# Optimization experiments

Hardware: AMD Instinct MI355X
Metric: run time of the kernel (lower is better)

## Reference

```python
import jax, jax.numpy as jnp
import numpy as np

OUT_F, IN_F = 8192, 4096
TOKENS = 512


def _unpack_int2_to_ternary(packed, alpha, dtype):
    # packed: [out_f, in_f//4] ints 0..255; 4 two-bit codes per byte.
    # code 0 -> -1, code 2 -> +1, codes 1/3 -> 0; then scale by per-row alpha.
    shifts = jnp.arange(4, dtype=packed.dtype) * 2  # [0,2,4,6]
    two_bit = (packed[:, :, None] >> shifts[None, None, :]) & 3  # [out_f, in_f//4, 4]
    two_bit = two_bit.reshape(packed.shape[0], -1)  # [out_f, in_f]
    sign = jnp.where(two_bit == 2, 1.0, jnp.where(two_bit == 0, -1.0, 0.0)).astype(dtype)
    return sign * alpha.astype(dtype)[:, None]


def setup_inputs() -> dict:
    key = jax.random.key(0)
    k1, k2, k3, k4 = jax.random.split(key, 4)
    x = jax.random.normal(k1, (TOKENS, IN_F), dtype=jnp.float32)
    weight_int2 = jax.random.randint(k2, (OUT_F, IN_F // 4), 0, 256, dtype=jnp.int32)
    alpha = jax.random.uniform(k3, (OUT_F,), dtype=jnp.float32, minval=0.01, maxval=0.05)
    bias = jax.random.normal(k4, (OUT_F,), dtype=jnp.float32) * 0.01
    return {"x": x, "weight_int2": weight_int2, "alpha": alpha, "bias": bias}


def reference(x, weight_int2, alpha, bias):
    W = _unpack_int2_to_ternary(weight_int2, alpha, x.dtype)  # [out_f, in_f]
    out = x @ W.T  # [tokens, out_f]
    return out + bias
```

## Files before the change

kernel.cpp:

```cpp
#include <hip/hip_runtime.h>
#include <hip/hip_bf16.h>

typedef unsigned int u32;
typedef unsigned short u16;

#define TOKENS 512
#define OUT_F  8192
#define IN_F   4096
#define KPACK  (IN_F / 4)

#define TM 128
#define TN 64
#define BK 64
#define LDK 72

typedef __attribute__((ext_vector_type(8))) short bf16x8;
typedef __attribute__((ext_vector_type(4))) float f32x4;

__device__ __forceinline__ u32 pack_bf16x2(float a, float b) {
    __hip_bfloat162 h = __float22bfloat162_rn(make_float2(a, b));
    union { __hip_bfloat162 h2; u32 u; } cvt;
    cvt.h2 = h;
    return cvt.u;
}

__device__ __forceinline__ void decode4(u32 w, u32& lo, u32& hi) {
    u32 t = (w & 0xFFu) * 0x4001u;
    u32 u = t >> 4;
    u32 nt = ~t;
    u32 nu = ~u;
    lo = ((nt & 0x10001u) * 0x3F80u) | ((nt & 0x20002u) << 14);
    hi = ((nu & 0x10001u) * 0x3F80u) | ((nu & 0x20002u) << 14);
}

__global__ __launch_bounds__(256, 2) void ternary_gemm(
    const float* __restrict__ X,
    const u32* __restrict__ W2,
    const float* __restrict__ alpha,
    const float* __restrict__ bias,
    float* __restrict__ Out)
{
    __shared__ u16 As[TM * LDK];
    __shared__ u16 Bs[TN * LDK];

    const int tid  = threadIdx.x;
    const int lane = tid & 63;
    const int wave = tid >> 6;
    const int quad = lane >> 4;
    const int lr   = lane & 15;

    const int n0 = blockIdx.x * TN;
    const int m0 = blockIdx.y * TM;

    const int wm = (wave >> 1) * 64;
    const int wn = (wave & 1) * 32;

    f32x4 acc[4][2];
#pragma unroll
    for (int i = 0; i < 4; ++i)
#pragma unroll
        for (int j = 0; j < 2; ++j)
            acc[i][j] = (f32x4){0.f, 0.f, 0.f, 0.f};

    const int bn = tid >> 2;
    const int bq = tid & 3;

    float4 aregs[8];
    uint4 breg;

#pragma unroll
    for (int r = 0; r < 4; ++r) {
        int idx = r * 256 + tid;
        int m = idx >> 3, c = idx & 7;
        const float* p = X + (m0 + m) * IN_F + c * 8;
        aregs[2 * r]     = *(const float4*)(p);
        aregs[2 * r + 1] = *(const float4*)(p + 4);
    }
    breg = *(const uint4*)(W2 + (n0 + bn) * KPACK + bq * 4);

    for (int ks = 0; ks < IN_F; ks += BK) {
        __syncthreads();

#pragma unroll
        for (int r = 0; r < 4; ++r) {
            int idx = r * 256 + tid;
            int m = idx >> 3, c = idx & 7;
            float4 fa = aregs[2 * r], fb = aregs[2 * r + 1];
            uint4 q;
            q.x = pack_bf16x2(fa.x, fa.y);
            q.y = pack_bf16x2(fa.z, fa.w);
            q.z = pack_bf16x2(fb.x, fb.y);
            q.w = pack_bf16x2(fb.z, fb.w);
            *(uint4*)(As + m * LDK + c * 8) = q;
        }
        {
            u32 w0 = breg.x, w1 = breg.y, w2v = breg.z, w3 = breg.w;
            u32 o0, o1, o2, o3, o4, o5, o6, o7;
            decode4(w0, o0, o1);
            decode4(w1, o2, o3);
            decode4(w2v, o4, o5);
            decode4(w3, o6, o7);
            uint4 lo = {o0, o1, o2, o3};
            uint4 hi = {o4, o5, o6, o7};
            *(uint4*)(Bs + bn * LDK + bq * 16)     = lo;
            *(uint4*)(Bs + bn * LDK + bq * 16 + 8) = hi;
        }

        if (ks + BK < IN_F) {
            int ks2 = ks + BK;
#pragma unroll
            for (int r = 0; r < 4; ++r) {
                int idx = r * 256 + tid;
                int m = idx >> 3, c = idx & 7;
                const float* p = X + (m0 + m) * IN_F + ks2 + c * 8;
                aregs[2 * r]     = *(const float4*)(p);
                aregs[2 * r + 1] = *(const float4*)(p + 4);
            }
            breg = *(const uint4*)(W2 + (n0 + bn) * KPACK + (ks2 >> 2) + bq * 4);
        }

        __syncthreads();

#pragma unroll
        for (int kk = 0; kk < 2; ++kk) {
            bf16x8 afrag[4], bfrag[2];
#pragma unroll
            for (int mt = 0; mt < 4; ++mt)
                afrag[mt] = *(const bf16x8*)(As + (wm + mt * 16 + lr) * LDK + kk * 32 + quad * 8);
#pragma unroll
            for (int nt = 0; nt < 2; ++nt)
                bfrag[nt] = *(const bf16x8*)(Bs + (wn + nt * 16 + lr) * LDK + kk * 32 + quad * 8);
#pragma unroll
            for (int mt = 0; mt < 4; ++mt)
#pragma unroll
                for (int nt = 0; nt < 2; ++nt)
                    acc[mt][nt] = __builtin_amdgcn_mfma_f32_16x16x32_bf16(
                        afrag[mt], bfrag[nt], acc[mt][nt], 0, 0, 0);
        }
    }

#pragma unroll
    for (int nt = 0; nt < 2; ++nt) {
        int ncol = n0 + wn + nt * 16 + lr;
        float av = alpha[ncol];
        float bv = bias[ncol];
#pragma unroll
        for (int mt = 0; mt < 4; ++mt) {
            int mbase = m0 + wm + mt * 16 + quad * 4;
#pragma unroll
            for (int r = 0; r < 4; ++r) {
                Out[(mbase + r) * OUT_F + ncol] = acc[mt][nt][r] * av + bv;
            }
        }
    }
}

extern "C" void kernel_launch(void* const* d_in, const int* in_sizes, int n_in,
                              void* d_out, int out_size, void* d_ws, size_t ws_size,
                              hipStream_t stream) {
    const float* x = (const float*)d_in[0];
    const u32* w2 = (const u32*)d_in[1];
    const float* alpha = (const float*)d_in[2];
    const float* bias  = (const float*)d_in[3];
    float* out = (float*)d_out;

    dim3 grid(OUT_F / TN, TOKENS / TM);
    ternary_gemm<<<grid, 256, 0, stream>>>(x, w2, alpha, bias, out);
}
```

Before: 150.4 us.

## Drop LDS staging, load MFMA fragments from global, decode weights via LUT

Adds a pre-pass that converts X to bf16 in the workspace. The GEMM then loads A and B fragments directly from global memory into registers with double buffering, instead of staging them through shared memory with two barriers per k-step. Weight bytes are decoded through a 256-entry shared LUT rather than arithmetic. This removes the LDS round trips and synchronisation, but the direct global fragment loads are less coalesced, each operand is re-read by several waves rather than shared, and there is an extra kernel launch.

```diff
diff --git a/kernel.cpp b/kernel.cpp
--- a/kernel.cpp
+++ b/kernel.cpp
@@ -12,7 +12,6 @@
 #define TM 128
 #define TN 64
 #define BK 64
-#define LDK 72
 
 typedef __attribute__((ext_vector_type(8))) short bf16x8;
 typedef __attribute__((ext_vector_type(4))) float f32x4;
@@ -33,15 +32,29 @@
     hi = ((nu & 0x10001u) * 0x3F80u) | ((nu & 0x20002u) << 14);
 }
 
+__global__ __launch_bounds__(256) void convert_x(const float* __restrict__ X,
+                                                 u16* __restrict__ Xb) {
+    int i = (blockIdx.x * 256 + threadIdx.x) * 8;
+    float4 a = *(const float4*)(X + i);
+    float4 b = *(const float4*)(X + i + 4);
+    uint4 q;
+    q.x = pack_bf16x2(a.x, a.y);
+    q.y = pack_bf16x2(a.z, a.w);
+    q.z = pack_bf16x2(b.x, b.y);
+    q.w = pack_bf16x2(b.z, b.w);
+    *(uint4*)(Xb + i) = q;
+}
+
+template <bool PRE>
 __global__ __launch_bounds__(256, 2) void ternary_gemm(
-    const float* __restrict__ X,
+    const float* __restrict__ Xf,
+    const u16* __restrict__ Xb,
     const u32* __restrict__ W2,
     const float* __restrict__ alpha,
     const float* __restrict__ bias,
     float* __restrict__ Out)
 {
-    __shared__ u16 As[TM * LDK];
-    __shared__ u16 Bs[TN * LDK];
+    __shared__ uint2 LUT[256];
 
     const int tid  = threadIdx.x;
     const int lane = tid & 63;
@@ -49,9 +62,15 @@
     const int quad = lane >> 4;
     const int lr   = lane & 15;
 
+    {
+        u32 lo, hi;
+        decode4((u32)tid, lo, hi);
+        LUT[tid] = make_uint2(lo, hi);
+    }
+    __syncthreads();
+
     const int n0 = blockIdx.x * TN;
     const int m0 = blockIdx.y * TM;
-
     const int wm = (wave >> 1) * 64;
     const int wn = (wave & 1) * 32;
 
@@ -62,81 +81,72 @@
         for (int j = 0; j < 2; ++j)
             acc[i][j] = (f32x4){0.f, 0.f, 0.f, 0.f};
 
-    const int bn = tid >> 2;
-    const int bq = tid & 3;
+    auto load_a = [&](int ks, bf16x8* af) {
+#pragma unroll
+        for (int mt = 0; mt < 4; ++mt) {
+            int row = m0 + wm + mt * 16 + lr;
+#pragma unroll
+            for (int kk = 0; kk < 2; ++kk) {
+                int k = ks + kk * 32 + quad * 8;
+                if (PRE) {
+                    af[mt * 2 + kk] = *(const bf16x8*)(Xb + (size_t)row * IN_F + k);
+                } else {
+                    const float* p = Xf + (size_t)row * IN_F + k;
+                    float4 fa = *(const float4*)p;
+                    float4 fb = *(const float4*)(p + 4);
+                    union { bf16x8 v; u32 u[4]; } c;
+                    c.u[0] = pack_bf16x2(fa.x, fa.y);
+                    c.u[1] = pack_bf16x2(fa.z, fa.w);
+                    c.u[2] = pack_bf16x2(fb.x, fb.y);
+                    c.u[3] = pack_bf16x2(fb.z, fb.w);
+                    af[mt * 2 + kk] = c.v;
+                }
+            }
+        }
+    };
 
-    float4 aregs[8];
-    uint4 breg;
+    auto load_b = [&](int ks, uint2* br) {
+#pragma unroll
+        for (int nt = 0; nt < 2; ++nt) {
+            const u32* rp = W2 + (size_t)(n0 + wn + nt * 16 + lr) * KPACK
+                               + (ks >> 2) + quad * 2;
+            br[nt * 2 + 0] = *(const uint2*)(rp);
+            br[nt * 2 + 1] = *(const uint2*)(rp + 8);
+        }
+    };
 
+    auto compute = [&](const bf16x8* af, const uint2* br) {
 #pragma unroll
-    for (int r = 0; r < 4; ++r) {
-        int idx = r * 256 + tid;
-        int m = idx >> 3, c = idx & 7;
-        const float* p = X + (m0 + m) * IN_F + c * 8;
-        aregs[2 * r]     = *(const float4*)(p);
-        aregs[2 * r + 1] = *(const float4*)(p + 4);
-    }
-    breg = *(const uint4*)(W2 + (n0 + bn) * KPACK + bq * 4);
+        for (int nt = 0; nt < 2; ++nt) {
+#pragma unroll
+            for (int kk = 0; kk < 2; ++kk) {
+                uint2 g = br[nt * 2 + kk];
+                union { bf16x8 v; uint2 u[2]; } bf;
+                bf.u[0] = LUT[g.x & 0xFFu];
+                bf.u[1] = LUT[g.y & 0xFFu];
+#pragma unroll
+                for (int mt = 0; mt < 4; ++mt)
+                    acc[mt][nt] = __builtin_amdgcn_mfma_f32_16x16x32_bf16(
+                        af[mt * 2 + kk], bf.v, acc[mt][nt], 0, 0, 0);
+            }
+        }
+    };
 
-    for (int ks = 0; ks < IN_F; ks += BK) {
-        __syncthreads();
+    bf16x8 afA[8], afB[8];
+    uint2  brA[4], brB[4];
 
-#pragma unroll
-        for (int r = 0; r < 4; ++r) {
-            int idx = r * 256 + tid;
-            int m = idx >> 3, c = idx & 7;
-            float4 fa = aregs[2 * r], fb = aregs[2 * r + 1];
-            uint4 q;
-            q.x = pack_bf16x2(fa.x, fa.y);
-            q.y = pack_bf16x2(fa.z, fa.w);
-            q.z = pack_bf16x2(fb.x, fb.y);
-            q.w = pack_bf16x2(fb.z, fb.w);
-            *(uint4*)(As + m * LDK + c * 8) = q;
+    load_a(0, afA);
+    load_b(0, brA);
+
+    for (int ks = 0; ks < IN_F; ks += 2 * BK) {
+        load_a(ks + BK, afB);
+        load_b(ks + BK, brB);
+        compute(afA, brA);
+        if (ks + 2 * BK < IN_F) {
+            load_a(ks + 2 * BK, afA);
+            load_b(ks + 2 * BK, brA);
         }
-        {
-            u32 w0 = breg.x, w1 = breg.y, w2v = breg.z, w3 = breg.w;
-            u32 o0, o1, o2, o3, o4, o5, o6, o7;
-            decode4(w0, o0, o1);
-            decode4(w1, o2, o3);
-            decode4(w2v, o4, o5);
-            decode4(w3, o6, o7);
-            uint4 lo = {o0, o1, o2, o3};
-            uint4 hi = {o4, o5, o6, o7};
-            *(uint4*)(Bs + bn * LDK + bq * 16)     = lo;
-            *(uint4*)(Bs + bn * LDK + bq * 16 + 8) = hi;
-        }
-
-        if (ks + BK < IN_F) {
-            int ks2 = ks + BK;
-#pragma unroll
-            for (int r = 0; r < 4; ++r) {
-                int idx = r * 256 + tid;
-                int m = idx >> 3, c = idx & 7;
-                const float* p = X + (m0 + m) * IN_F + ks2 + c * 8;
-                aregs[2 * r]     = *(const float4*)(p);
-                aregs[2 * r + 1] = *(const float4*)(p + 4);
-            }
-            breg = *(const uint4*)(W2 + (n0 + bn) * KPACK + (ks2 >> 2) + bq * 4);
-        }
-
-        __syncthreads();
-
-#pragma unroll
-        for (int kk = 0; kk < 2; ++kk) {
-            bf16x8 afrag[4], bfrag[2];
-#pragma unroll
-            for (int mt = 0; mt < 4; ++mt)
-                afrag[mt] = *(const bf16x8*)(As + (wm + mt * 16 + lr) * LDK + kk * 32 + quad * 8);
-#pragma unroll
-            for (int nt = 0; nt < 2; ++nt)
-                bfrag[nt] = *(const bf16x8*)(Bs + (wn + nt * 16 + lr) * LDK + kk * 32 + quad * 8);
-#pragma unroll
-            for (int mt = 0; mt < 4; ++mt)
-#pragma unroll
-                for (int nt = 0; nt < 2; ++nt)
-                    acc[mt][nt] = __builtin_amdgcn_mfma_f32_16x16x32_bf16(
-                        afrag[mt], bfrag[nt], acc[mt][nt], 0, 0, 0);
-        }
+        compute(afB, brB);
     }
 
 #pragma unroll
@@ -149,7 +159,7 @@
             int mbase = m0 + wm + mt * 16 + quad * 4;
 #pragma unroll
             for (int r = 0; r < 4; ++r) {
-                Out[(mbase + r) * OUT_F + ncol] = acc[mt][nt][r] * av + bv;
+                Out[(size_t)(mbase + r) * OUT_F + ncol] = acc[mt][nt][r] * av + bv;
             }
         }
     }
@@ -165,5 +175,13 @@
     float* out = (float*)d_out;
 
     dim3 grid(OUT_F / TN, TOKENS / TM);
-    ternary_gemm<<<grid, 256, 0, stream>>>(x, w2, alpha, bias, out);
+
+    const size_t need = (size_t)TOKENS * IN_F * sizeof(u16);
+    if (ws_size >= need) {
+        u16* xb = (u16*)d_ws;
+        convert_x<<<(TOKENS * IN_F) / (256 * 8), 256, 0, stream>>>(x, xb);
+        ternary_gemm<true><<<grid, 256, 0, stream>>>(x, xb, w2, alpha, bias, out);
+    } else {
+        ternary_gemm<false><<<grid, 256, 0, stream>>>(x, nullptr, w2, alpha, bias, out);
+    }
 }
```

Result: slower. 253.1 us (+68.3%).
